# Kernel optimization log

Hardware: AMD Instinct MI355X
Metric: run time of the kernel (lower is better)

## Reference

```python
import jax, jax.numpy as jnp
import numpy as np

B, C, H, W = 8, 96, 224, 224
WS, SS, NH = 7, 3, 3          # window size, shift size, num heads
HD = C // NH                  # head dim = 32
N = WS * WS                   # tokens per window = 49
MLP_H = 4 * C
EPS = 1e-5


def _rel_pos_index():
    coords = np.stack(np.meshgrid(np.arange(WS), np.arange(WS), indexing='ij'))  # (2, ws, ws)
    cf = coords.reshape(2, -1)                       # (2, N)
    rel = cf[:, :, None] - cf[:, None, :]            # (2, N, N)
    rel = rel.transpose(1, 2, 0).copy()              # (N, N, 2)
    rel[:, :, 0] += WS - 1
    rel[:, :, 1] += WS - 1
    rel[:, :, 0] *= 2 * WS - 1
    return rel.sum(-1)                               # (N, N) int


def _attn_mask():
    # Swin shifted-window mask: (num_windows, N, N) with 0 / -100
    img = np.zeros((H, W), np.float32)
    cnt = 0
    for hs in (slice(0, -WS), slice(-WS, -SS), slice(-SS, None)):
        for ws_ in (slice(0, -WS), slice(-WS, -SS), slice(-SS, None)):
            img[hs, ws_] = cnt
            cnt += 1
    mw = img.reshape(H // WS, WS, W // WS, WS).transpose(0, 2, 1, 3).reshape(-1, N)
    m = mw[:, None, :] - mw[:, :, None]
    return np.where(m != 0, np.float32(-100.0), np.float32(0.0))


def setup_inputs() -> dict:
    key = jax.random.key(0)
    ks = jax.random.split(key, 8)
    s = 0.02
    return {
        "x": jax.random.normal(ks[0], (B, C, H, W), jnp.float32),
        "attn_mask": jnp.asarray(_attn_mask()),
        "norm1_g": jnp.ones((C,), jnp.float32),
        "norm1_b": jnp.zeros((C,), jnp.float32),
        "qkv_w": jax.random.normal(ks[1], (C, 3 * C), jnp.float32) * s,
        "qkv_b": jnp.zeros((3 * C,), jnp.float32),
        "rpb": jax.random.normal(ks[2], ((2 * WS - 1) ** 2, NH), jnp.float32) * s,
        "proj_w": jax.random.normal(ks[3], (C, C), jnp.float32) * s,
        "proj_b": jnp.zeros((C,), jnp.float32),
        "norm2_g": jnp.ones((C,), jnp.float32),
        "norm2_b": jnp.zeros((C,), jnp.float32),
        "fc1_w": jax.random.normal(ks[4], (C, MLP_H), jnp.float32) * s,
        "fc1_b": jnp.zeros((MLP_H,), jnp.float32),
        "fc2_w": jax.random.normal(ks[5], (MLP_H, C), jnp.float32) * s,
        "fc2_b": jnp.zeros((C,), jnp.float32),
    }


def _ln(x, g, b):
    mu = jnp.mean(x, axis=-1, keepdims=True)
    var = jnp.var(x, axis=-1, keepdims=True)
    return (x - mu) * jax.lax.rsqrt(var + EPS) * g + b


def reference(x, attn_mask, norm1_g, norm1_b, qkv_w, qkv_b, rpb, proj_w, proj_b,
              norm2_g, norm2_b, fc1_w, fc1_b, fc2_w, fc2_b):
    shortcut = x
    # (B,C,H,W) -> (B,HW,C) -> LN -> (B,H,W,C)
    xl = jnp.transpose(x, (0, 2, 3, 1)).reshape(B, H * W, C)
    xl = _ln(xl, norm1_g, norm1_b).reshape(B, H, W, C)
    # H,W divisible by WS: pad_r = pad_b = 0
    sx = jnp.roll(xl, (-SS, -SS), axis=(1, 2))
    # window partition -> (B*nW, N, C)
    xw = sx.reshape(B, H // WS, WS, W // WS, WS, C).transpose(0, 1, 3, 2, 4, 5).reshape(-1, N, C)
    B_ = xw.shape[0]
    nW = B_ // B
    qkv = (xw @ qkv_w + qkv_b).reshape(B_, N, 3, NH, HD).transpose(2, 0, 3, 1, 4)
    q = qkv[0] * (HD ** -0.5)
    k, v = qkv[1], qkv[2]
    attn = jnp.einsum('bhnd,bhmd->bhnm', q, k)           # (B_, NH, N, N)
    rel_idx = jnp.asarray(_rel_pos_index())
    bias = rpb[rel_idx.reshape(-1)].reshape(N, N, NH).transpose(2, 0, 1)  # (NH, N, N)
    attn = attn + bias[None]
    attn = attn.reshape(B, nW, NH, N, N) + attn_mask[None, :, None]
    attn = jax.nn.softmax(attn.reshape(B_, NH, N, N), axis=-1)
    out = jnp.einsum('bhnm,bhmd->bhnd', attn, v).transpose(0, 2, 1, 3).reshape(B_, N, C)
    out = out @ proj_w + proj_b
    # window reverse -> (B, H, W, C)
    out = out.reshape(B, H // WS, W // WS, WS, WS, C).transpose(0, 1, 3, 2, 4, 5).reshape(B, H, W, C)
    out = jnp.roll(out, (SS, SS), axis=(1, 2))
    # faithful to original: permute(0,1,3,2) then raw reshape to (B,C,H,W)
    out = jnp.transpose(out, (0, 1, 3, 2)).reshape(B, C, H, W)
    x1 = shortcut + out
    # MLP branch, faithful: permute(0,1,3,2) then raw reshape to (B,HW,C)
    xm = jnp.transpose(x1, (0, 1, 3, 2)).reshape(B, H * W, C)
    xm = _ln(xm, norm2_g, norm2_b)
    xm = jax.nn.gelu(xm @ fc1_w + fc1_b, approximate=False) @ fc2_w + fc2_b
    xm = xm.reshape(B, C, H, W)
    return x1 + xm
```

## Files before the change

### kernel.cpp

```cpp
#include <hip/hip_runtime.h>
#include <hip/hip_bf16.h>


typedef __attribute__((ext_vector_type(4))) float f32x4;
typedef __attribute__((ext_vector_type(8))) short s16x8;

constexpr int B_ = 8;
constexpr int M_ = 96 * 224 * 224;

__device__ __forceinline__ ushort f2bs(float f) {
    __hip_bfloat16 h = __float2bfloat16(f);
    ushort u; __builtin_memcpy(&u, &h, 2); return u;
}
__device__ __forceinline__ float bs2f(ushort u) {
    __hip_bfloat16 h; __builtin_memcpy(&h, &u, 2); return __bfloat162float(h);
}
__device__ __forceinline__ f32x4 mfma16(s16x8 a, s16x8 b, f32x4 c) {
    return __builtin_amdgcn_mfma_f32_16x16x32_bf16(a, b, c, 0, 0, 0);
}
__device__ __forceinline__ float gelu_f(float v) {
    float s  = v * 0.70710678118654752f;
    float as = fabsf(s);
    float t  = __builtin_amdgcn_rcpf(fmaf(0.3275911f, as, 1.0f));
    float p  = fmaf(fmaf(fmaf(fmaf(1.061405429f, t, -1.453152027f), t,
                   1.421413741f), t, -0.284496736f), t, 0.254829592f) * t;
    float y  = 1.0f - p * __expf(-s * s);
    float er = copysignf(y, s);
    return 0.5f * v * (1.0f + er);
}

__global__ __launch_bounds__(256) void prep_kernel(
    const float* __restrict__ qkvw, const float* __restrict__ projw,
    const float* __restrict__ w1,   const float* __restrict__ w2,
    ushort* __restrict__ wq, ushort* __restrict__ wp,
    ushort* __restrict__ wf1, ushort* __restrict__ wf2)
{
    int i = blockIdx.x * 256 + threadIdx.x;
    if (i < 27648) { int n = i / 96, k = i % 96;  wq[i]  = f2bs(qkvw[k * 288 + n]); }
    if (i < 9216)  { int n = i / 96, k = i % 96;  wp[i]  = f2bs(projw[k * 96 + n]); }
    if (i < 36864) {
        int n = i / 96,  k = i % 96;   wf1[i] = f2bs(w1[k * 384 + n]);
        int n2 = i / 384, k2 = i % 384; wf2[i] = f2bs(w2[k2 * 96 + n2]);
    }
}

__global__ __launch_bounds__(256) void attn_kernel(
    const float* __restrict__ x,
    const float* __restrict__ amask,
    const float* __restrict__ n1g, const float* __restrict__ n1b,
    const float* __restrict__ qkvb,
    const float* __restrict__ rpb,
    const float* __restrict__ projb,
    const ushort* __restrict__ wq, const ushort* __restrict__ wp,
    ushort* __restrict__ x1)
{
    __shared__ __align__(16) ushort T[64][104];
    __shared__ __align__(16) ushort K[64][104];
    __shared__ __align__(16) ushort vT[96][72];
    __shared__ __align__(16) ushort Pws[4][16][72];
    __shared__ float rpbs[512];

    const int tid  = threadIdx.x;
    const int wave = tid >> 6, lane = tid & 63;
    const int cu   = lane & 15;
    const int g4   = lane >> 4;
    const int gk8  = g4 << 3;
    const int gr4  = g4 << 2;

    const int blk = (blockIdx.x & 7) * 1024 + (blockIdx.x >> 3);
    const int b   = blk >> 10;
    const int wi  = blk & 1023;
    const int wh  = wi >> 5, ww = wi & 31;
    const int bM  = b * M_;
    const bool need_mask = (wh == 31) || (ww == 31);

    for (int i = tid; i < 507; i += 256) rpbs[i] = rpb[i];

    const int t49 = tid % 49;
    const int g5  = tid / 49;
    int hh_s = 0, wc_s = 0;
    if (tid < 245) {
        int i = t49 / 7, j = t49 % 7;
        hh_s = wh * 7 + i + 3; if (hh_s >= 224) hh_s -= 224;
        wc_s = ww * 7 + j + 3; if (wc_s >= 224) wc_s -= 224;
    }

    if (tid < 245) {
        const float* xp = x + bM + g5 * 50176 + hh_s * 224 + wc_s;
        ushort* dT = &T[t49][g5];
        for (int c = g5; c < 96; c += 5) {
            *dT = f2bs(*xp);
            xp += 5 * 50176; dT += 5;
        }
    }
    {
        uint* z = (uint*)&T[49][0];
        for (int i = tid; i < 780; i += 256) z[i] = 0u;
    }
    __syncthreads();

    if (tid < 196) {
        int t = tid >> 2, s = tid & 3;
        float sum = 0.f, sq = 0.f;
        float vv[24];
        #pragma unroll
        for (int i = 0; i < 24; ++i) {
            vv[i] = bs2f(T[t][s * 24 + i]);
            sum += vv[i]; sq += vv[i] * vv[i];
        }
        sum += __shfl_xor(sum, 1); sq += __shfl_xor(sq, 1);
        sum += __shfl_xor(sum, 2); sq += __shfl_xor(sq, 2);
        float mu   = sum * (1.0f / 96.0f);
        float rstd = rsqrtf(sq * (1.0f / 96.0f) - mu * mu + 1e-5f);
        #pragma unroll
        for (int i = 0; i < 24; ++i) {
            int c = s * 24 + i;
            T[t][c] = f2bs((vv[i] - mu) * rstd * n1g[c] + n1b[c]);
        }
    }
    __syncthreads();

    const int ar = (wave << 4) | cu;
    const int tr = (wave << 4) + gr4;

    {
        s16x8 a0 = *(const s16x8*)&T[ar][gk8];
        s16x8 a1 = *(const s16x8*)&T[ar][32 + gk8];
        s16x8 a2 = *(const s16x8*)&T[ar][64 + gk8];
        f32x4 qreg[6];
        #pragma unroll
        for (int nt = 0; nt < 18; ++nt) {
            int nc = (nt << 4) | cu;
            const ushort* bp = wq + nc * 96 + gk8;
            s16x8 b0 = *(const s16x8*)(bp);
            s16x8 b1 = *(const s16x8*)(bp + 32);
            s16x8 b2 = *(const s16x8*)(bp + 64);
            f32x4 acc = {0.f, 0.f, 0.f, 0.f};
            acc = mfma16(a0, b0, acc);
            acc = mfma16(a1, b1, acc);
            acc = mfma16(a2, b2, acc);
            float bias = qkvb[nc];
            if (nt < 6) {
                #pragma unroll
                for (int r = 0; r < 4; ++r)
                    qreg[nt][r] = (acc[r] + bias) * 0.17677669529663689f;
            } else if (nc < 192) {
                #pragma unroll
                for (int r = 0; r < 4; ++r) K[tr + r][nc - 96] = f2bs(acc[r] + bias);
            } else {
                int d = nc - 192;
                ushort4 pk;
                pk.x = f2bs(acc[0] + bias); pk.y = f2bs(acc[1] + bias);
                pk.z = f2bs(acc[2] + bias); pk.w = f2bs(acc[3] + bias);
                *(ushort4*)&vT[d][tr] = pk;
            }
        }
        #pragma unroll
        for (int qn = 0; qn < 6; ++qn)
            #pragma unroll
            for (int r = 0; r < 4; ++r)
                T[tr + r][(qn << 4) | cu] = f2bs(qreg[qn][r]);
    }
    __syncthreads();

    int u7d[4], u7m[4];
    #pragma unroll
    for (int ut = 0; ut < 4; ++ut) {
        int u = (ut << 4) | cu;
        u7d[ut] = u / 7; u7m[ut] = u % 7;
    }

    f32x4 osc[3][2];
    #pragma unroll
    for (int it = 0; it < 3; ++it) {
        const int hh = it;
        const int t0r = tr;

        s16x8 aq = *(const s16x8*)&T[ar][(hh << 5) + gk8];
        f32x4 sa[4];
        #pragma unroll
        for (int ut = 0; ut < 4; ++ut) {
            s16x8 bk = *(const s16x8*)&K[(ut << 4) | cu][(hh << 5) + gk8];
            f32x4 z = {0.f, 0.f, 0.f, 0.f};
            sa[ut] = mfma16(aq, bk, z);
        }
        #pragma unroll
        for (int ut = 0; ut < 4; ++ut) {
            int u = (ut << 4) | cu;
            #pragma unroll
            for (int r = 0; r < 4; ++r) {
                int t = t0r + r;
                float s = sa[ut][r];
                if (t < 49 && u < 49) {
                    int dr = t / 7 - u7d[ut] + 6, dc = t % 7 - u7m[ut] + 6;
                    s += rpbs[(dr * 13 + dc) * 3 + hh];
                    if (need_mask) s += amask[(wi * 49 + t) * 49 + u];
                } else if (u >= 49) {
                    s = -1e30f;
                }
                sa[ut][r] = s;
            }
        }
        float inv[4];
        #pragma unroll
        for (int r = 0; r < 4; ++r) {
            float m = fmaxf(fmaxf(sa[0][r], sa[1][r]), fmaxf(sa[2][r], sa[3][r]));
            m = fmaxf(m, __shfl_xor(m, 1)); m = fmaxf(m, __shfl_xor(m, 2));
            m = fmaxf(m, __shfl_xor(m, 4)); m = fmaxf(m, __shfl_xor(m, 8));
            float e0 = __expf(sa[0][r] - m), e1 = __expf(sa[1][r] - m);
            float e2 = __expf(sa[2][r] - m), e3 = __expf(sa[3][r] - m);
            sa[0][r] = e0; sa[1][r] = e1; sa[2][r] = e2; sa[3][r] = e3;
            float s = (e0 + e1) + (e2 + e3);
            s += __shfl_xor(s, 1); s += __shfl_xor(s, 2);
            s += __shfl_xor(s, 4); s += __shfl_xor(s, 8);
            inv[r] = 1.0f / s;
        }
        #pragma unroll
        for (int ut = 0; ut < 4; ++ut) {
            int u = (ut << 4) | cu;
            #pragma unroll
            for (int r = 0; r < 4; ++r) Pws[wave][gr4 + r][u] = f2bs(sa[ut][r]);
        }
        s16x8 pa0 = *(const s16x8*)&Pws[wave][cu][gk8];
        s16x8 pa1 = *(const s16x8*)&Pws[wave][cu][32 + gk8];
        #pragma unroll
        for (int nt = 0; nt < 2; ++nt) {
            int d = (hh << 5) + (nt << 4) + cu;
            s16x8 bv0 = *(const s16x8*)&vT[d][gk8];
            s16x8 bv1 = *(const s16x8*)&vT[d][32 + gk8];
            f32x4 acc = {0.f, 0.f, 0.f, 0.f};
            acc = mfma16(pa0, bv0, acc);
            acc = mfma16(pa1, bv1, acc);
            #pragma unroll
            for (int r = 0; r < 4; ++r) osc[it][nt][r] = acc[r] * inv[r];
        }
    }
    __syncthreads();

    #pragma unroll
    for (int it = 0; it < 3; ++it)
        #pragma unroll
        for (int nt = 0; nt < 2; ++nt)
            #pragma unroll
            for (int r = 0; r < 4; ++r)
                K[tr + r][(it << 5) + (nt << 4) + cu] = f2bs(osc[it][nt][r]);

    {
        s16x8 a0 = *(const s16x8*)&K[ar][gk8];
        s16x8 a1 = *(const s16x8*)&K[ar][32 + gk8];
        s16x8 a2 = *(const s16x8*)&K[ar][64 + gk8];
        #pragma unroll
        for (int nt = 0; nt < 6; ++nt) {
            int nc = (nt << 4) | cu;
            const ushort* bp = wp + nc * 96 + gk8;
            s16x8 b0 = *(const s16x8*)(bp);
            s16x8 b1 = *(const s16x8*)(bp + 32);
            s16x8 b2 = *(const s16x8*)(bp + 64);
            f32x4 acc = {0.f, 0.f, 0.f, 0.f};
            acc = mfma16(a0, b0, acc);
            acc = mfma16(a1, b1, acc);
            acc = mfma16(a2, b2, acc);
            float bias = projb[nc];
            #pragma unroll
            for (int r = 0; r < 4; ++r) T[tr + r][nc] = f2bs(acc[r] + bias);
        }
    }
    __syncthreads();

    if (tid < 245) {
        const int base = bM + (hh_s * 96 + g5) * 224 + wc_s;
        const float* xp = x + base;
        ushort* dx = x1 + base;
        const ushort* Tp = &T[t49][g5];
        for (int c = g5; c < 96; c += 5) {
            *dx = f2bs(*xp + bs2f(*Tp));
            xp += 5 * 224; dx += 5 * 224; Tp += 5;
        }
    }
}

__global__ __launch_bounds__(256) void transpose_kernel(
    const ushort* __restrict__ x1, ushort* __restrict__ x1p)
{
    __shared__ ushort tile[32][36];
    const int id      = blockIdx.x;
    const int tile_id = id % 49;
    const int slab    = id / 49;
    const int h0 = (tile_id / 7) * 32;
    const int w0 = (tile_id % 7) * 32;
    const ushort* src = x1  + slab * 50176;
    ushort*       dst = x1p + slab * 50176;

    const int i = threadIdx.x >> 3;
    const int j = (threadIdx.x & 7) * 4;

    *(ushort4*)&tile[i][j] = *(const ushort4*)&src[(h0 + i) * 224 + w0 + j];
    __syncthreads();
    ushort4 v;
    v.x = tile[j][i]; v.y = tile[j + 1][i]; v.z = tile[j + 2][i]; v.w = tile[j + 3][i];
    *(ushort4*)&dst[(w0 + i) * 224 + h0 + j] = v;
}

template <bool CLEAN>
__device__ __forceinline__ void ln_token(
    const ushort* __restrict__ xsrc, int tok, int gk8,
    const float* __restrict__ n2g, const float* __restrict__ n2b,
    s16x8& a0, s16x8& a1, s16x8& a2)
{
    float vals[24];
    if (CLEAN) {
        const ushort* base = xsrc + tok * 96 + gk8;
        s16x8 r0 = *(const s16x8*)(base);
        s16x8 r1 = *(const s16x8*)(base + 32);
        s16x8 r2 = *(const s16x8*)(base + 64);
        #pragma unroll
        for (int i = 0; i < 8; ++i) {
            vals[i]      = bs2f((ushort)r0[i]);
            vals[8 + i]  = bs2f((ushort)r1[i]);
            vals[16 + i] = bs2f((ushort)r2[i]);
        }
    } else {
        int bb = tok / 50176;
        int tl = tok % 50176;
        #pragma unroll
        for (int s = 0; s < 3; ++s)
            #pragma unroll
            for (int i = 0; i < 8; ++i) {
                int p = tl * 96 + gk8 + s * 32 + i;
                int c = p / 50176, rem = p % 50176;
                int w = rem / 224, h = rem % 224;
                vals[s * 8 + i] = bs2f(xsrc[bb * M_ + c * 50176 + h * 224 + w]);
            }
    }
    float sum = 0.f, sq = 0.f;
    #pragma unroll
    for (int i = 0; i < 24; ++i) { sum += vals[i]; sq += vals[i] * vals[i]; }
    sum += __shfl_xor(sum, 16); sq += __shfl_xor(sq, 16);
    sum += __shfl_xor(sum, 32); sq += __shfl_xor(sq, 32);
    float mu   = sum * (1.0f / 96.0f);
    float rstd = rsqrtf(sq * (1.0f / 96.0f) - mu * mu + 1e-5f);
    #pragma unroll
    for (int i = 0; i < 8; ++i) {
        int c0 = gk8 + i, c1 = gk8 + 32 + i, c2 = gk8 + 64 + i;
        a0[i] = (short)f2bs((vals[i]      - mu) * rstd * n2g[c0] + n2b[c0]);
        a1[i] = (short)f2bs((vals[8 + i]  - mu) * rstd * n2g[c1] + n2b[c1]);
        a2[i] = (short)f2bs((vals[16 + i] - mu) * rstd * n2g[c2] + n2b[c2]);
    }
}

template <bool CLEAN>
__global__ __launch_bounds__(256) void mlp_kernel(
    const ushort* __restrict__ xsrc,
    const ushort* __restrict__ x1flat,
    const float* __restrict__ n2g, const float* __restrict__ n2b,
    const float* __restrict__ b1v, const float* __restrict__ b2v,
    const ushort* __restrict__ wf1, const ushort* __restrict__ wf2,
    float* __restrict__ out)
{
    __shared__ __align__(16) ushort hS[4][2][32][40];

    const int tid  = threadIdx.x;
    const int wave = tid >> 6, lane = tid & 63;
    const int cu   = lane & 15;
    const int g4   = lane >> 4;
    const int gk8  = g4 << 3;
    const int gr4  = g4 << 2;
    const int t0g  = blockIdx.x * 128;
    const int tokA = t0g + (wave << 5) + cu;
    const int tokB = tokA + 16;

    s16x8 aA0, aA1, aA2, aB0, aB1, aB2;
    ln_token<CLEAN>(xsrc, tokA, gk8, n2g, n2b, aA0, aA1, aA2);
    ln_token<CLEAN>(xsrc, tokB, gk8, n2g, n2b, aB0, aB1, aB2);

    auto fc1_step = [&](int s, int buf) {
        #pragma unroll
        for (int half = 0; half < 2; ++half) {
            int nc = ((2 * s + half) << 4) | cu;
            const ushort* bp = wf1 + nc * 96 + gk8;
            s16x8 b0 = *(const s16x8*)(bp);
            s16x8 b1 = *(const s16x8*)(bp + 32);
            s16x8 b2 = *(const s16x8*)(bp + 64);
            float bias = b1v[nc];
            f32x4 accA = {0.f, 0.f, 0.f, 0.f};
            accA = mfma16(aA0, b0, accA);
            accA = mfma16(aA1, b1, accA);
            accA = mfma16(aA2, b2, accA);
            f32x4 accB = {0.f, 0.f, 0.f, 0.f};
            accB = mfma16(aB0, b0, accB);
            accB = mfma16(aB1, b1, accB);
            accB = mfma16(aB2, b2, accB);
            #pragma unroll
            for (int r = 0; r < 4; ++r) {
                hS[wave][buf][gr4 + r][(half << 4) | cu]      = f2bs(gelu_f(accA[r] + bias));
                hS[wave][buf][16 + gr4 + r][(half << 4) | cu] = f2bs(gelu_f(accB[r] + bias));
            }
        }
    };

    f32x4 oaccA[6], oaccB[6];
    #pragma unroll
    for (int nt2 = 0; nt2 < 6; ++nt2) {
        oaccA[nt2] = (f32x4){0.f, 0.f, 0.f, 0.f};
        oaccB[nt2] = (f32x4){0.f, 0.f, 0.f, 0.f};
    }

    fc1_step(0, 0);
    for (int s = 0; s < 12; ++s) {
        int buf = s & 1;
        s16x8 haA = *(const s16x8*)&hS[wave][buf][cu][gk8];
        s16x8 haB = *(const s16x8*)&hS[wave][buf][16 + cu][gk8];
        if (s < 11) fc1_step(s + 1, buf ^ 1);
        #pragma unroll
        for (int nt2 = 0; nt2 < 6; ++nt2) {
            int nc2 = (nt2 << 4) | cu;
            s16x8 bv = *(const s16x8*)&wf2[nc2 * 384 + s * 32 + gk8];
            oaccA[nt2] = mfma16(haA, bv, oaccA[nt2]);
            oaccB[nt2] = mfma16(haB, bv, oaccB[nt2]);
        }
    }

    const int trow = (wave << 5) + gr4;
    #pragma unroll
    for (int nt2 = 0; nt2 < 6; ++nt2) {
        int nc2 = (nt2 << 4) | cu;
        float bias = b2v[nc2];
        #pragma unroll
        for (int r = 0; r < 4; ++r) {
            int GA = (t0g + trow + r) * 96 + nc2;
            out[GA] = bias + oaccA[nt2][r] + bs2f(x1flat[GA]);
            int GB = GA + 16 * 96;
            out[GB] = bias + oaccB[nt2][r] + bs2f(x1flat[GB]);
        }
    }
}

extern "C" void kernel_launch(void* const* d_in, const int* in_sizes, int n_in,
                              void* d_out, int out_size, void* d_ws, size_t ws_size,
                              hipStream_t stream) {
    const float* x      = (const float*)d_in[0];
    const float* amask  = (const float*)d_in[1];
    const float* n1g    = (const float*)d_in[2];
    const float* n1b    = (const float*)d_in[3];
    const float* qkvw   = (const float*)d_in[4];
    const float* qkvb   = (const float*)d_in[5];
    const float* rpb    = (const float*)d_in[6];
    const float* projw  = (const float*)d_in[7];
    const float* projb  = (const float*)d_in[8];
    const float* n2g    = (const float*)d_in[9];
    const float* n2b    = (const float*)d_in[10];
    const float* w1     = (const float*)d_in[11];
    const float* b1     = (const float*)d_in[12];
    const float* w2     = (const float*)d_in[13];
    const float* b2     = (const float*)d_in[14];

    char* ws = (char*)d_ws;
    ushort* wq  = (ushort*)(ws);
    ushort* wp  = (ushort*)(ws + 55296);
    ushort* wf1 = (ushort*)(ws + 73728);
    ushort* wf2 = (ushort*)(ws + 147456);
    ushort* x1  = (ushort*)(ws + 262144);
    ushort* x1p = (ushort*)(ws + 77332480);
    float* out = (float*)d_out;

    const bool clean = (ws_size >= (size_t)154402816);

    prep_kernel<<<dim3(144), dim3(256), 0, stream>>>(qkvw, projw, w1, w2, wq, wp, wf1, wf2);

    attn_kernel<<<dim3(8192), dim3(256), 0, stream>>>(
        x, amask, n1g, n1b, qkvb, rpb, projb, wq, wp, x1);

    if (clean) {
        transpose_kernel<<<dim3(37632), dim3(256), 0, stream>>>(x1, x1p);
        mlp_kernel<true><<<dim3(3136), dim3(256), 0, stream>>>(
            x1p, x1, n2g, n2b, b1, b2, wf1, wf2, out);
    } else {
        mlp_kernel<false><<<dim3(3136), dim3(256), 0, stream>>>(
            x1, x1, n2g, n2b, b1, b2, wf1, wf2, out);
    }
}
```

Before: 646.2 us.

## Fuse residual add and transpose into attention epilogue, dropping transpose kernel

The attention kernel now writes the attention output straight into the T tile and feeds it to the projection GEMM, which removes the osc staging registers and one block barrier. The projection epilogue adds the residual directly from global x. It writes x1 and also scatters a transposed copy into x1p, so the separate transpose kernel launch and its full read/write pass are gone. In exchange the stores are scattered, single-element and less coalesced, and when no clean workspace exists x1p aliases x1, which causes duplicate writes. Writing T while other waves may still read T for q could be a race, since the barrier that used to separate them was removed.

```diff
diff --git a/kernel.cpp b/kernel.cpp
--- a/kernel.cpp
+++ b/kernel.cpp
@@ -52,7 +52,7 @@
     const float* __restrict__ rpb,
     const float* __restrict__ projb,
     const ushort* __restrict__ wq, const ushort* __restrict__ wp,
-    ushort* __restrict__ x1)
+    ushort* __restrict__ x1, ushort* __restrict__ x1p)
 {
     __shared__ __align__(16) ushort T[64][104];
     __shared__ __align__(16) ushort K[64][104];
@@ -170,7 +170,6 @@
         u7d[ut] = u / 7; u7m[ut] = u % 7;
     }
 
-    f32x4 osc[3][2];
     #pragma unroll
     for (int it = 0; it < 3; ++it) {
         const int hh = it;
@@ -232,23 +231,32 @@
             acc = mfma16(pa0, bv0, acc);
             acc = mfma16(pa1, bv1, acc);
             #pragma unroll
-            for (int r = 0; r < 4; ++r) osc[it][nt][r] = acc[r] * inv[r];
-        }
-    }
-    __syncthreads();
-
-    #pragma unroll
-    for (int it = 0; it < 3; ++it)
-        #pragma unroll
-        for (int nt = 0; nt < 2; ++nt)
-            #pragma unroll
             for (int r = 0; r < 4; ++r)
-                K[tr + r][(it << 5) + (nt << 4) + cu] = f2bs(osc[it][nt][r]);
+                T[t0r + r][(hh << 5) + (nt << 4) + cu] = f2bs(acc[r] * inv[r]);
+        }
+    }
 
     {
-        s16x8 a0 = *(const s16x8*)&K[ar][gk8];
-        s16x8 a1 = *(const s16x8*)&K[ar][32 + gk8];
-        s16x8 a2 = *(const s16x8*)&K[ar][64 + gk8];
+        s16x8 a0 = *(const s16x8*)&T[ar][gk8];
+        s16x8 a1 = *(const s16x8*)&T[ar][32 + gk8];
+        s16x8 a2 = *(const s16x8*)&T[ar][64 + gk8];
+
+        int f1v[4], q224[4], r224[4], wv[4];
+        bool val[4];
+        #pragma unroll
+        for (int r = 0; r < 4; ++r) {
+            int t = tr + r;
+            val[r] = (t < 49);
+            int i = t / 7, j = t % 7;
+            int h = wh * 7 + i + 3; if (h >= 224) h -= 224;
+            int w = ww * 7 + j + 3; if (w >= 224) w -= 224;
+            int HC = h * 96 + cu;
+            q224[r] = HC / 224;
+            r224[r] = HC - q224[r] * 224;
+            wv[r]   = w;
+            f1v[r]  = bM + HC * 224 + w;
+        }
+
         #pragma unroll
         for (int nt = 0; nt < 6; ++nt) {
             int nc = (nt << 4) | cu;
@@ -262,43 +270,19 @@
             acc = mfma16(a2, b2, acc);
             float bias = projb[nc];
             #pragma unroll
-            for (int r = 0; r < 4; ++r) T[tr + r][nc] = f2bs(acc[r] + bias);
-        }
-    }
-    __syncthreads();
-
-    if (tid < 245) {
-        const int base = bM + (hh_s * 96 + g5) * 224 + wc_s;
-        const float* xp = x + base;
-        ushort* dx = x1 + base;
-        const ushort* Tp = &T[t49][g5];
-        for (int c = g5; c < 96; c += 5) {
-            *dx = f2bs(*xp + bs2f(*Tp));
-            xp += 5 * 224; dx += 5 * 224; Tp += 5;
-        }
-    }
-}
-
-__global__ __launch_bounds__(256) void transpose_kernel(
-    const ushort* __restrict__ x1, ushort* __restrict__ x1p)
-{
-    __shared__ ushort tile[32][36];
-    const int id      = blockIdx.x;
-    const int tile_id = id % 49;
-    const int slab    = id / 49;
-    const int h0 = (tile_id / 7) * 32;
-    const int w0 = (tile_id % 7) * 32;
-    const ushort* src = x1  + slab * 50176;
-    ushort*       dst = x1p + slab * 50176;
-
-    const int i = threadIdx.x >> 3;
-    const int j = (threadIdx.x & 7) * 4;
-
-    *(ushort4*)&tile[i][j] = *(const ushort4*)&src[(h0 + i) * 224 + w0 + j];
-    __syncthreads();
-    ushort4 v;
-    v.x = tile[j][i]; v.y = tile[j + 1][i]; v.z = tile[j + 2][i]; v.w = tile[j + 3][i];
-    *(ushort4*)&dst[(w0 + i) * 224 + h0 + j] = v;
+            for (int r = 0; r < 4; ++r) {
+                if (val[r]) {
+                    float y = acc[r] + bias + x[f1v[r]];
+                    ushort yb = f2bs(y);
+                    x1[f1v[r]] = yb;
+                    x1p[bM + q224[r] * 50176 + wv[r] * 224 + r224[r]] = yb;
+                }
+                f1v[r] += 16 * 224;
+                r224[r] += 16;
+                if (r224[r] >= 224) { r224[r] -= 224; q224[r] += 1; }
+            }
+        }
+    }
 }
 
 template <bool CLEAN>
@@ -467,14 +451,14 @@
 
     prep_kernel<<<dim3(144), dim3(256), 0, stream>>>(qkvw, projw, w1, w2, wq, wp, wf1, wf2);
 
-    attn_kernel<<<dim3(8192), dim3(256), 0, stream>>>(
-        x, amask, n1g, n1b, qkvb, rpb, projb, wq, wp, x1);
-
     if (clean) {
-        transpose_kernel<<<dim3(37632), dim3(256), 0, stream>>>(x1, x1p);
+        attn_kernel<<<dim3(8192), dim3(256), 0, stream>>>(
+            x, amask, n1g, n1b, qkvb, rpb, projb, wq, wp, x1, x1p);
         mlp_kernel<true><<<dim3(3136), dim3(256), 0, stream>>>(
             x1p, x1, n2g, n2b, b1, b2, wf1, wf2, out);
     } else {
+        attn_kernel<<<dim3(8192), dim3(256), 0, stream>>>(
+            x, amask, n1g, n1b, qkvb, rpb, projb, wq, wp, x1, x1);
         mlp_kernel<false><<<dim3(3136), dim3(256), 0, stream>>>(
             x1, x1, n2g, n2b, b1, b2, wf1, wf2, out);
     }
```

Result: slower. 747.0 us (+15.6%).
